# Kernel tuning notes

Hardware: AMD Instinct MI355X
Metric: run time of the kernel (lower is better)

The kernel has to match this reference:

```python
import jax, jax.numpy as jnp
import numpy as np

N, E, G = 100000, 300000, 4096
ND, ED, H, ZI, ZS, NE, L = 64, 16, 256, 128, 128, 8, 3
LAMBDA_GRL = 1.0


def setup_inputs() -> dict:
    key = jax.random.key(0)
    ks = iter(jax.random.split(key, 64))
    def nrm(shape, scale=0.05):
        return jax.random.normal(next(ks), shape, jnp.float32) * scale
    inp = {
        'x': jax.random.normal(next(ks), (N, ND), jnp.float32),
        'edge_index': jax.random.randint(next(ks), (2, E), 0, N),
        'edge_attr': jax.random.normal(next(ks), (E, ED), jnp.float32),
        'batch': jnp.sort(jax.random.randint(next(ks), (N,), 0, G)),
        'node_W': nrm((ND, H)), 'node_b': nrm((H,)),
        'conv_eps': jnp.zeros((L,), jnp.float32),
        'edge_W': nrm((L, ED, H)), 'edge_b': nrm((L, H)),
        'mlp_W1': nrm((L, H, H)), 'mlp_b1': nrm((L, H)),
        'mlp_W2': nrm((L, H, H)), 'mlp_b2': nrm((L, H)),
        'gn_w': jnp.ones((L, H), jnp.float32), 'gn_b': jnp.zeros((L, H), jnp.float32),
        'gn_ms': jnp.ones((L, H), jnp.float32),
        'finv_W1': nrm((H, ZI)), 'finv_b1': nrm((ZI,)),
        'finv_W2': nrm((ZI, ZI)), 'finv_b2': nrm((ZI,)),
        'fspu_W1': nrm((H, ZS)), 'fspu_b1': nrm((ZS,)),
        'fspu_W2': nrm((ZS, ZS)), 'fspu_b2': nrm((ZS,)),
        'pred_W1': nrm((ZI, ZI)), 'pred_b1': nrm((ZI,)),
        'pred_W2': nrm((ZI, 1)), 'pred_b2': nrm((1,)),
        'adv_W1': nrm((ZI, ZI)), 'adv_b1': nrm((ZI,)),
        'adv_W2': nrm((ZI, NE)), 'adv_b2': nrm((NE,)),
    }
    return inp


def _mlp2(h, W1, b1, W2, b2):
    return jax.nn.relu(h @ W1 + b1) @ W2 + b2


def reference(x, edge_index, edge_attr, batch, node_W, node_b, conv_eps,
              edge_W, edge_b, mlp_W1, mlp_b1, mlp_W2, mlp_b2,
              gn_w, gn_b, gn_ms,
              finv_W1, finv_b1, finv_W2, finv_b2,
              fspu_W1, fspu_b1, fspu_W2, fspu_b2,
              pred_W1, pred_b1, pred_W2, pred_b2,
              adv_W1, adv_b1, adv_W2, adv_b2):
    src, dst = edge_index[0], edge_index[1]
    cnt = jax.ops.segment_sum(jnp.ones((N, 1), jnp.float32), batch, num_segments=G)
    cnt = jnp.maximum(cnt, 1.0)
    h = x @ node_W + node_b  # [N,H]
    for l in range(L):
        # GINEConv: sum_j relu(x_j + lin(e_ij))
        e = edge_attr @ edge_W[l] + edge_b[l]            # [E,H]
        m = jax.nn.relu(h[src] + e)                      # [E,H]
        agg = jax.ops.segment_sum(m, dst, num_segments=N)
        h = _mlp2((1.0 + conv_eps[l]) * h + agg, mlp_W1[l], mlp_b1[l], mlp_W2[l], mlp_b2[l])
        # GraphNorm
        mean = jax.ops.segment_sum(h, batch, num_segments=G) / cnt  # [G,H]
        out = h - gn_ms[l] * mean[batch]
        var = jax.ops.segment_sum(out * out, batch, num_segments=G) / cnt
        h = out * jax.lax.rsqrt(var[batch] + 1e-5) * gn_w[l] + gn_b[l]
        h = jax.nn.relu(h)  # dropout is identity at eval
    hg = jax.ops.segment_sum(h, batch, num_segments=G) / cnt  # global_mean_pool [G,H]
    z_inv = _mlp2(hg, finv_W1, finv_b1, finv_W2, finv_b2)
    z_spu = _mlp2(hg, fspu_W1, fspu_b1, fspu_W2, fspu_b2)
    yhat = _mlp2(z_inv, pred_W1, pred_b1, pred_W2, pred_b2)[:, 0]
    # gradient reversal: identity fwd, -lambda on bwd
    grl = jax.lax.stop_gradient(z_inv) * (1.0 + LAMBDA_GRL) - LAMBDA_GRL * z_inv
    envhat = _mlp2(grl, adv_W1, adv_b1, adv_W2, adv_b2)
    return (hg, z_inv, z_spu, yhat, envhat)
```

## Files before the change

kernel.cpp:

```cpp
#include <hip/hip_runtime.h>
#include <hip/hip_bf16.h>

typedef __bf16 bf16_t;
typedef __bf16 bf16x8 __attribute__((ext_vector_type(8)));
typedef __bf16 bf16x4 __attribute__((ext_vector_type(4)));
typedef float  f32x4  __attribute__((ext_vector_type(4)));

static constexpr int N_NODES = 100000;
static constexpr int N_EDGES = 300000;
static constexpr int N_GRAPH = 4096;
static constexpr int H  = 256;
static constexpr int ND = 64;
static constexpr int ZIC = 128;
static constexpr int NE = 8;
static constexpr int SCAN_B = 1024;

__device__ __forceinline__ int clampi(int v, int lo, int hi) {
  return v < lo ? lo : (v > hi ? hi : v);
}

__device__ __forceinline__ void dma16(const bf16_t* g, bf16_t* lds_base) {
  __builtin_amdgcn_global_load_lds(
      (const __attribute__((address_space(1))) void*)g,
      (__attribute__((address_space(3))) void*)lds_base, 16, 0, 0);
}

__global__ void compute_starts_kernel(const int* __restrict__ batch,
                                      int* __restrict__ starts, int N, int G) {
  int i = blockIdx.x * blockDim.x + threadIdx.x;
  if (i >= N) return;
  int b = clampi(batch[i], 0, G - 1);
  if (i == 0) {
    for (int g = 0; g <= b; ++g) starts[g] = 0;
  } else {
    int p = clampi(batch[i - 1], 0, G - 1);
    for (int g = p + 1; g <= b; ++g) starts[g] = i;
  }
  if (i == N - 1) {
    for (int g = b + 1; g <= G; ++g) starts[g] = N;
  }
}

__global__ void zero2_kernel(int* __restrict__ a, int* __restrict__ b, int N) {
  int i = blockIdx.x * blockDim.x + threadIdx.x;
  if (i < N) { a[i] = 0; b[i] = 0; }
}

__global__ void count_deg_kernel(const int* __restrict__ dst, int* __restrict__ counts, int E, int N) {
  int e = blockIdx.x * blockDim.x + threadIdx.x;
  if (e < E) atomicAdd(&counts[clampi(dst[e], 0, N - 1)], 1);
}

__global__ __launch_bounds__(SCAN_B) void scan1_kernel(const int* __restrict__ counts,
                                                       int* __restrict__ offs,
                                                       int* __restrict__ bsum, int N) {
  __shared__ int tmp[SCAN_B];
  int i = blockIdx.x * SCAN_B + threadIdx.x;
  int v = (i < N) ? counts[i] : 0;
  tmp[threadIdx.x] = v;
  __syncthreads();
  for (int d = 1; d < SCAN_B; d <<= 1) {
    int t = (threadIdx.x >= d) ? tmp[threadIdx.x - d] : 0;
    __syncthreads();
    tmp[threadIdx.x] += t;
    __syncthreads();
  }
  if (i < N) offs[i + 1] = tmp[threadIdx.x];
  if (threadIdx.x == SCAN_B - 1) bsum[blockIdx.x] = tmp[SCAN_B - 1];
  if (i == 0) offs[0] = 0;
}

__global__ void scan2_kernel(int* __restrict__ bsum, int nblk) {
  if (blockIdx.x == 0 && threadIdx.x == 0) {
    int run = 0;
    for (int b = 0; b < nblk; ++b) { int v = bsum[b]; bsum[b] = run; run += v; }
  }
}

__global__ __launch_bounds__(SCAN_B) void scan3_kernel(int* __restrict__ offs,
                                                       const int* __restrict__ bsum, int N) {
  int i = blockIdx.x * SCAN_B + threadIdx.x;
  if (i < N) offs[i + 1] += bsum[blockIdx.x];
}

__global__ void fill_scatter_kernel(const int* __restrict__ src, const int* __restrict__ dst,
                                    const float* __restrict__ eattr,
                                    const int* __restrict__ offs, int* __restrict__ cursor,
                                    int* __restrict__ src_srt, bf16_t* __restrict__ eat16,
                                    int E, int N) {
  int e = blockIdx.x * blockDim.x + threadIdx.x;
  if (e >= E) return;
  int d = clampi(dst[e], 0, N - 1);
  int pos = offs[d] + atomicAdd(&cursor[d], 1);
  if ((unsigned)pos >= (unsigned)E) return;
  int s = src[e];
  src_srt[pos] = ((unsigned)s < (unsigned)N_NODES) ? s : 0;
  const float* ea = eattr + (size_t)e * 16;
  union { bf16_t b[16]; uint4 u[2]; } pk;
#pragma unroll
  for (int k = 0; k < 16; ++k) pk.b[k] = (bf16_t)ea[k];
  uint4* dst16 = (uint4*)(eat16 + ((size_t)pos << 4));
  dst16[0] = pk.u[0];
  dst16[1] = pk.u[1];
}

__global__ void build_ewt16_kernel(const float* __restrict__ edge_W,
                                   bf16_t* __restrict__ ewt) {
  int idx = blockIdx.x * blockDim.x + threadIdx.x;
  if (idx >= 3 * 256 * 16) return;
  int l = idx / (256 * 16);
  int rem = idx - l * 256 * 16;
  int n = rem >> 4, k = rem & 15;
  ewt[idx] = (bf16_t)edge_W[(size_t)l * 16 * 256 + k * 256 + n];
}

__global__ void transpose_kernel(const float* __restrict__ W,
                                 bf16_t* __restrict__ Wt, int K, int Nc,
                                 size_t srcStride, size_t dstStride) {
  __shared__ float tile[32][33];
  const float* Wz = W + (size_t)blockIdx.z * srcStride;
  bf16_t* Wtz = Wt + (size_t)blockIdx.z * dstStride;
  int n0 = blockIdx.x * 32, k0 = blockIdx.y * 32;
  int tx = threadIdx.x, ty = threadIdx.y;
  for (int i = ty; i < 32; i += 8)
    tile[i][tx] = Wz[(size_t)(k0 + i) * Nc + n0 + tx];
  __syncthreads();
  for (int i = ty; i < 32; i += 8)
    Wtz[(size_t)(n0 + i) * K + k0 + tx] = (bf16_t)tile[tx][i];
}

__device__ __forceinline__ void load8_to_lds(const bf16_t* p, bool valid, uint4* dst) {
  uint4 v = make_uint4(0u, 0u, 0u, 0u);
  if (valid) v = *(const uint4*)p;
  *dst = v;
}
__device__ __forceinline__ void load8_to_lds(const float* p, bool valid, uint4* dst) {
  float4 f0 = make_float4(0.f, 0.f, 0.f, 0.f), f1 = f0;
  if (valid) { f0 = *(const float4*)p; f1 = *(const float4*)(p + 4); }
  union { bf16_t b[8]; uint4 u; } pk;
  pk.b[0] = (bf16_t)f0.x; pk.b[1] = (bf16_t)f0.y;
  pk.b[2] = (bf16_t)f0.z; pk.b[3] = (bf16_t)f0.w;
  pk.b[4] = (bf16_t)f1.x; pk.b[5] = (bf16_t)f1.y;
  pk.b[6] = (bf16_t)f1.z; pk.b[7] = (bf16_t)f1.w;
  *dst = pk.u;
}

template<int K, bool RELU, bool OUTF32, typename TIN>
__global__ __launch_bounds__(256) void gemm128_kernel(
    const TIN* __restrict__ U, const bf16_t* __restrict__ Wt,
    const float* __restrict__ bias, void* __restrict__ Out, int M, int Nc) {
  constexpr int LDT = 72;
  __shared__ bf16_t Ut[128 * LDT];
  __shared__ bf16_t Wl[128 * LDT];
  const int m0 = blockIdx.x * 128;
  const int n0 = blockIdx.y * 128;
  const int t = threadIdx.x;
  const int lane = t & 63;
  const int wave = t >> 6;
  const int wm = (wave >> 1) * 64;
  const int wn = (wave & 1) * 64;
  const int srow = t >> 1;
  const int sk = (t & 1) * 32;
  const int lr = lane & 15;
  const int lq = lane >> 4;
  const bool aok = (m0 + srow) < M;
  f32x4 acc[4][4] = {};

  for (int k0 = 0; k0 < K; k0 += 64) {
    const TIN* up = U + (size_t)(m0 + srow) * K + k0 + sk;
    const bf16_t* wp = Wt + (size_t)(n0 + srow) * K + k0 + sk;
#pragma unroll
    for (int q = 0; q < 4; ++q) {
      load8_to_lds(up + q * 8, aok, (uint4*)&Ut[srow * LDT + sk + q * 8]);
      load8_to_lds(wp + q * 8, true, (uint4*)&Wl[srow * LDT + sk + q * 8]);
    }
    __syncthreads();
#pragma unroll
    for (int s = 0; s < 2; ++s) {
      bf16x8 a[4], b[4];
#pragma unroll
      for (int mt = 0; mt < 4; ++mt)
        a[mt] = *(const bf16x8*)(&Ut[(wm + mt * 16 + lr) * LDT + s * 32 + lq * 8]);
#pragma unroll
      for (int nt = 0; nt < 4; ++nt)
        b[nt] = *(const bf16x8*)(&Wl[(wn + nt * 16 + lr) * LDT + s * 32 + lq * 8]);
#pragma unroll
      for (int mt = 0; mt < 4; ++mt)
#pragma unroll
        for (int nt = 0; nt < 4; ++nt)
          acc[mt][nt] = __builtin_amdgcn_mfma_f32_16x16x32_bf16(
              a[mt], b[nt], acc[mt][nt], 0, 0, 0);
    }
    __syncthreads();
  }

#pragma unroll
  for (int mt = 0; mt < 4; ++mt)
#pragma unroll
    for (int nt = 0; nt < 4; ++nt) {
      int col = n0 + wn + nt * 16 + lr;
      float bcol = bias[col];
#pragma unroll
      for (int r = 0; r < 4; ++r) {
        int row = m0 + wm + mt * 16 + lq * 4 + r;
        if (row < M) {
          float vv = acc[mt][nt][r] + bcol;
          if (RELU) vv = vv > 0.f ? vv : 0.f;
          if (OUTF32) ((float*)Out)[(size_t)row * Nc + col] = vv;
          else        ((bf16_t*)Out)[(size_t)row * Nc + col] = (bf16_t)vv;
        }
      }
    }
}

template<int K, bool RELU, bool OUTF32, typename TIN>
__global__ __launch_bounds__(256) void gemm64_kernel(
    const TIN* __restrict__ U, const bf16_t* __restrict__ Wt,
    const float* __restrict__ bias, void* __restrict__ Out, int M, int Nc) {
  constexpr int LDT = 72;
  __shared__ bf16_t Ut[64 * LDT];
  __shared__ bf16_t Wl[64 * LDT];
  const int m0 = blockIdx.x * 64;
  const int n0 = blockIdx.y * 64;
  const int t = threadIdx.x;
  const int lane = t & 63;
  const int wave = t >> 6;
  const int wm = (wave >> 1) * 32;
  const int wn = (wave & 1) * 32;
  const int srow = t >> 2;
  const int sk = (t & 3) * 8;
  const int lr = lane & 15;
  const int lq = lane >> 4;
  const bool aok = (m0 + srow) < M;
  f32x4 acc[2][2] = {};

  for (int k0 = 0; k0 < K; k0 += 64) {
    const TIN* up = U + (size_t)(m0 + srow) * K + k0 + sk;
    const bf16_t* wp = Wt + (size_t)(n0 + srow) * K + k0 + sk;
    load8_to_lds(up,      aok, (uint4*)&Ut[srow * LDT + sk]);
    load8_to_lds(up + 32, aok, (uint4*)&Ut[srow * LDT + sk + 32]);
    load8_to_lds(wp,      true, (uint4*)&Wl[srow * LDT + sk]);
    load8_to_lds(wp + 32, true, (uint4*)&Wl[srow * LDT + sk + 32]);
    __syncthreads();
#pragma unroll
    for (int s = 0; s < 2; ++s) {
      bf16x8 a[2], b[2];
#pragma unroll
      for (int mt = 0; mt < 2; ++mt)
        a[mt] = *(const bf16x8*)(&Ut[(wm + mt * 16 + lr) * LDT + s * 32 + lq * 8]);
#pragma unroll
      for (int nt = 0; nt < 2; ++nt)
        b[nt] = *(const bf16x8*)(&Wl[(wn + nt * 16 + lr) * LDT + s * 32 + lq * 8]);
#pragma unroll
      for (int mt = 0; mt < 2; ++mt)
#pragma unroll
        for (int nt = 0; nt < 2; ++nt)
          acc[mt][nt] = __builtin_amdgcn_mfma_f32_16x16x32_bf16(
              a[mt], b[nt], acc[mt][nt], 0, 0, 0);
    }
    __syncthreads();
  }

#pragma unroll
  for (int mt = 0; mt < 2; ++mt)
#pragma unroll
    for (int nt = 0; nt < 2; ++nt) {
      int col = n0 + wn + nt * 16 + lr;
      float bcol = bias[col];
#pragma unroll
      for (int r = 0; r < 4; ++r) {
        int row = m0 + wm + mt * 16 + lq * 4 + r;
        if (row < M) {
          float vv = acc[mt][nt][r] + bcol;
          if (RELU) vv = vv > 0.f ? vv : 0.f;
          if (OUTF32) ((float*)Out)[(size_t)row * Nc + col] = vv;
          else        ((bf16_t*)Out)[(size_t)row * Nc + col] = (bf16_t)vv;
        }
      }
    }
}

template<int K, bool RELU, bool OUTF32>
__global__ __launch_bounds__(256) void gemm128_dma_kernel(
    const bf16_t* __restrict__ U, const bf16_t* __restrict__ Wt,
    const float* __restrict__ bias, void* __restrict__ Out, int M, int Nc) {
  __shared__ bf16_t Ut[128 * 64];
  __shared__ bf16_t Wl[128 * 64];
  const int t = threadIdx.x;
  const int lane = t & 63;
  const int wave = t >> 6;
  const int m0 = blockIdx.x * 128;
  const int n0 = blockIdx.y * 128;
  const int wm = (wave >> 1) * 64;
  const int wn = (wave & 1) * 64;
  const int lr = lane & 15;
  const int lq = lane >> 4;
  const int subrow = wave * 8 + (lane >> 3);
  const int lchunk = (lane & 7) ^ (lane >> 3);
  f32x4 acc[4][4] = {};

  for (int k0 = 0; k0 < K; k0 += 64) {
#pragma unroll
    for (int q = 0; q < 4; ++q) {
      const int row = q * 32 + subrow;
      int urow = m0 + row; if (urow >= M) urow = M - 1;
      dma16(U + (size_t)urow * K + k0 + lchunk * 8, &Ut[(q * 32 + wave * 8) * 64]);
      dma16(Wt + (size_t)(n0 + row) * K + k0 + lchunk * 8, &Wl[(q * 32 + wave * 8) * 64]);
    }
    __syncthreads();
#pragma unroll
    for (int s = 0; s < 2; ++s) {
      bf16x8 a[4], b[4];
#pragma unroll
      for (int mt = 0; mt < 4; ++mt)
        a[mt] = *(const bf16x8*)(&Ut[(wm + mt * 16 + lr) * 64 + (((s * 4 + lq) ^ (lr & 7)) << 3)]);
#pragma unroll
      for (int nt = 0; nt < 4; ++nt)
        b[nt] = *(const bf16x8*)(&Wl[(wn + nt * 16 + lr) * 64 + (((s * 4 + lq) ^ (lr & 7)) << 3)]);
#pragma unroll
      for (int mt = 0; mt < 4; ++mt)
#pragma unroll
        for (int nt = 0; nt < 4; ++nt)
          acc[mt][nt] = __builtin_amdgcn_mfma_f32_16x16x32_bf16(
              a[mt], b[nt], acc[mt][nt], 0, 0, 0);
    }
    __syncthreads();
  }

#pragma unroll
  for (int mt = 0; mt < 4; ++mt)
#pragma unroll
    for (int nt = 0; nt < 4; ++nt) {
      int col = n0 + wn + nt * 16 + lr;
      float bcol = bias[col];
#pragma unroll
      for (int r = 0; r < 4; ++r) {
        int row = m0 + wm + mt * 16 + lq * 4 + r;
        if (row < M) {
          float vv = acc[mt][nt][r] + bcol;
          if (RELU) vv = vv > 0.f ? vv : 0.f;
          if (OUTF32) ((float*)Out)[(size_t)row * Nc + col] = vv;
          else        ((bf16_t*)Out)[(size_t)row * Nc + col] = (bf16_t)vv;
        }
      }
    }
}

__global__ __launch_bounds__(256) void gine_gather_mfma_kernel(
    const bf16_t* __restrict__ h, const bf16_t* __restrict__ eat16,
    const int* __restrict__ src_sorted, const int* __restrict__ offs,
    const bf16_t* __restrict__ ewt, const float* __restrict__ eb,
    const float* __restrict__ eps_p, bf16_t* __restrict__ u) {
  constexpr int HP = H + 8;
  __shared__ bf16_t slin[2][16 * HP];
  const int t = threadIdx.x;
  const int wave = t >> 6;
  const int lane = t & 63;
  const int lr = lane & 15;
  const int lq = lane >> 4;
  const int lane4 = lane * 4;
  const int n0 = blockIdx.x * 4;
  const int nodeN = n0 + wave;

  bf16x4 hs = *(const bf16x4*)(h + (size_t)nodeN * H + lane4);

  bf16x8 bfrag[4];
#pragma unroll
  for (int nt = 0; nt < 4; ++nt) {
    bf16x8 bv = {};
    if (lq < 2)
      bv = *(const bf16x8*)(ewt + ((wave * 64 + nt * 16 + lr) << 4) + (lq << 3));
    bfrag[nt] = bv;
  }
  float ebv[4];
#pragma unroll
  for (int i = 0; i < 4; ++i) ebv[i] = eb[lane4 + i];

  int bs = offs[n0], be = offs[n0 + 4];
  bs = clampi(bs, 0, N_EDGES);
  be = clampi(be, bs, N_EDGES);
  int ns = offs[nodeN], ne = offs[nodeN + 1];
  ns = clampi(ns, bs, be);
  ne = clampi(ne, ns, be);

  float acc[4] = {0.f, 0.f, 0.f, 0.f};
  int parity = 0;

  for (int cb = bs; cb < be; cb += 16, parity ^= 1) {
    int arow = cb + lr;
    if (arow >= N_EDGES) arow = N_EDGES - 1;
    bf16x8 afrag = {};
    if (lq < 2)
      afrag = *(const bf16x8*)(eat16 + ((size_t)arow << 4) + (lq << 3));
    f32x4 c[4];
#pragma unroll
    for (int nt = 0; nt < 4; ++nt) {
      f32x4 z = {};
      c[nt] = __builtin_amdgcn_mfma_f32_16x16x32_bf16(afrag, bfrag[nt], z, 0, 0, 0);
    }
#pragma unroll
    for (int nt = 0; nt < 4; ++nt)
#pragma unroll
      for (int r = 0; r < 4; ++r)
        slin[parity][(lq * 4 + r) * HP + wave * 64 + nt * 16 + lr] = (bf16_t)c[nt][r];
    __syncthreads();
    int j0 = ns > cb ? ns : cb;
    int j1 = ne < cb + 16 ? ne : cb + 16;
    for (int jb = j0; jb < j1; jb += 4) {
      int sidx[4];
#pragma unroll
      for (int q = 0; q < 4; ++q) {
        int jj = jb + q; if (jj > j1 - 1) jj = j1 - 1;
        sidx[q] = src_sorted[jj];
      }
      bf16x4 hv[4];
#pragma unroll
      for (int q = 0; q < 4; ++q)
        hv[q] = *(const bf16x4*)(h + (size_t)sidx[q] * H + lane4);
#pragma unroll
      for (int q = 0; q < 4; ++q) {
        if (jb + q < j1) {
          bf16x4 lv = *(const bf16x4*)(&slin[parity][(jb + q - cb) * HP + lane4]);
#pragma unroll
          for (int i = 0; i < 4; ++i)
            acc[i] += fmaxf((float)hv[q][i] + (float)lv[i] + ebv[i], 0.f);
        }
      }
    }
  }

  const float sc = 1.0f + eps_p[0];
  union { bf16x4 v; uint2 b; } o;
#pragma unroll
  for (int i = 0; i < 4; ++i) o.v[i] = (bf16_t)(sc * (float)hs[i] + acc[i]);
  *(uint2*)(u + (size_t)nodeN * H + lane4) = o.b;
}

__global__ __launch_bounds__(64) void graphnorm_kernel(
    const bf16_t* __restrict__ v, bf16_t* __restrict__ hout,
    const int* __restrict__ starts,
    const float* __restrict__ w, const float* __restrict__ b,
    const float* __restrict__ ms, float* __restrict__ hg) {
  const int g = blockIdx.x;
  const int c0 = threadIdx.x * 4;
  int s = starts[g], e = starts[g + 1];
  s = clampi(s, 0, N_NODES);
  e = clampi(e, s, N_NODES);
  const float cnt = (float)((e - s) > 1 ? (e - s) : 1);
  float sx[4] = {0.f, 0.f, 0.f, 0.f}, sxx[4] = {0.f, 0.f, 0.f, 0.f};
  int i = s;
  for (; i + 4 <= e; i += 4) {
    bf16x4 xv[4];
#pragma unroll
    for (int q = 0; q < 4; ++q)
      xv[q] = *(const bf16x4*)(v + (size_t)(i + q) * H + c0);
#pragma unroll
    for (int q = 0; q < 4; ++q)
#pragma unroll
      for (int j = 0; j < 4; ++j) { float f = (float)xv[q][j]; sx[j] += f; sxx[j] += f * f; }
  }
  for (; i < e; ++i) {
    bf16x4 xv = *(const bf16x4*)(v + (size_t)i * H + c0);
#pragma unroll
    for (int j = 0; j < 4; ++j) { float f = (float)xv[j]; sx[j] += f; sxx[j] += f * f; }
  }
  float sub[4], inv[4], bb[4], psum[4] = {0.f, 0.f, 0.f, 0.f};
#pragma unroll
  for (int j = 0; j < 4; ++j) {
    float mean = sx[j] / cnt;
    sub[j] = ms[c0 + j] * mean;
    float var = sxx[j] / cnt - 2.f * sub[j] * mean + sub[j] * sub[j];
    var = fmaxf(var, 0.f);
    inv[j] = rsqrtf(var + 1e-5f) * w[c0 + j];
    bb[j] = b[c0 + j];
  }
  i = s;
  for (; i + 4 <= e; i += 4) {
    bf16x4 xv[4];
#pragma unroll
    for (int q = 0; q < 4; ++q)
      xv[q] = *(const bf16x4*)(v + (size_t)(i + q) * H + c0);
#pragma unroll
    for (int q = 0; q < 4; ++q) {
      union { bf16x4 o; uint2 u; } pk;
#pragma unroll
      for (int j = 0; j < 4; ++j) {
        float o = ((float)xv[q][j] - sub[j]) * inv[j] + bb[j];
        o = o > 0.f ? o : 0.f;
        psum[j] += o;
        pk.o[j] = (bf16_t)o;
      }
      *(uint2*)(hout + (size_t)(i + q) * H + c0) = pk.u;
    }
  }
  for (; i < e; ++i) {
    bf16x4 xv = *(const bf16x4*)(v + (size_t)i * H + c0);
    union { bf16x4 o; uint2 u; } pk;
#pragma unroll
    for (int j = 0; j < 4; ++j) {
      float o = ((float)xv[j] - sub[j]) * inv[j] + bb[j];
      o = o > 0.f ? o : 0.f;
      psum[j] += o;
      pk.o[j] = (bf16_t)o;
    }
    *(uint2*)(hout + (size_t)i * H + c0) = pk.u;
  }
  if (hg) {
#pragma unroll
    for (int j = 0; j < 4; ++j) hg[(size_t)g * H + c0 + j] = psum[j] / cnt;
  }
}

__global__ void head_out_kernel(const bf16_t* __restrict__ In, const float* __restrict__ W,
                                const float* __restrict__ bias, float* __restrict__ Out,
                                int M, int K, int Nc) {
  int idx = blockIdx.x * blockDim.x + threadIdx.x;
  if (idx >= M * Nc) return;
  int r = idx / Nc, n = idx - r * Nc;
  float acc = bias[n];
  const bf16_t* in = In + (size_t)r * K;
  for (int k = 0; k < K; ++k) acc += (float)in[k] * W[(size_t)k * Nc + n];
  Out[idx] = acc;
}

extern "C" void kernel_launch(void* const* d_in, const int* in_sizes, int n_in,
                              void* d_out, int out_size, void* d_ws, size_t ws_size,
                              hipStream_t stream) {
  (void)in_sizes; (void)n_in; (void)out_size; (void)ws_size;
  const float* x        = (const float*)d_in[0];
  const int*   eidx     = (const int*)d_in[1];
  const float* eattr    = (const float*)d_in[2];
  const int*   batch    = (const int*)d_in[3];
  const float* node_W   = (const float*)d_in[4];
  const float* node_b   = (const float*)d_in[5];
  const float* conv_eps = (const float*)d_in[6];
  const float* edge_W   = (const float*)d_in[7];
  const float* edge_b   = (const float*)d_in[8];
  const float* mlp_W1   = (const float*)d_in[9];
  const float* mlp_b1   = (const float*)d_in[10];
  const float* mlp_W2   = (const float*)d_in[11];
  const float* mlp_b2   = (const float*)d_in[12];
  const float* gn_w     = (const float*)d_in[13];
  const float* gn_b     = (const float*)d_in[14];
  const float* gn_ms    = (const float*)d_in[15];
  const float* finv_W1  = (const float*)d_in[16];
  const float* finv_b1  = (const float*)d_in[17];
  const float* finv_W2  = (const float*)d_in[18];
  const float* finv_b2  = (const float*)d_in[19];
  const float* fspu_W1  = (const float*)d_in[20];
  const float* fspu_b1  = (const float*)d_in[21];
  const float* fspu_W2  = (const float*)d_in[22];
  const float* fspu_b2  = (const float*)d_in[23];
  const float* pred_W1  = (const float*)d_in[24];
  const float* pred_b1  = (const float*)d_in[25];
  const float* pred_W2  = (const float*)d_in[26];
  const float* pred_b2  = (const float*)d_in[27];
  const float* adv_W1   = (const float*)d_in[28];
  const float* adv_b1   = (const float*)d_in[29];
  const float* adv_W2   = (const float*)d_in[30];
  const float* adv_b2   = (const float*)d_in[31];
  float* out = (float*)d_out;

  float* out_hg = out;
  float* out_zi = out + (size_t)N_GRAPH * H;
  float* out_zs = out_zi + (size_t)N_GRAPH * ZIC;
  float* out_yh = out_zs + (size_t)N_GRAPH * ZIC;
  float* out_ev = out_yh + N_GRAPH;

  char* wp = (char*)d_ws;
  auto alloc = [&](size_t bytes) { char* p = wp; wp += (bytes + 255) & ~(size_t)255; return p; };
  bf16_t* A        = (bf16_t*)alloc((size_t)N_NODES * H * 2);
  bf16_t* B        = (bf16_t*)alloc((size_t)N_NODES * H * 2);
  bf16_t* Wt       = (bf16_t*)alloc((size_t)(H * ND + 6 * H * H) * 2);
  bf16_t* WtH      = (bf16_t*)alloc((size_t)(2 * ZIC * H + 4 * ZIC * ZIC) * 2);
  bf16_t* ewt16    = (bf16_t*)alloc((size_t)3 * 256 * 16 * 2);
  bf16_t* eat16    = (bf16_t*)alloc((size_t)N_EDGES * 16 * 2);
  int*    starts   = (int*)alloc((size_t)(N_GRAPH + 1) * 4);
  int*    counts   = (int*)alloc((size_t)N_NODES * 4);
  int*    cursor   = (int*)alloc((size_t)N_NODES * 4);
  int*    offs     = (int*)alloc((size_t)(N_NODES + 1) * 4);
  int*    bsum     = (int*)alloc((size_t)SCAN_B * 4);
  int*    src_srt  = (int*)alloc((size_t)N_EDGES * 4);
  bf16_t* tmp1     = (bf16_t*)alloc((size_t)N_GRAPH * ZIC * 2);
  bf16_t* tmp2     = (bf16_t*)alloc((size_t)N_GRAPH * ZIC * 2);

  const int* srcp = eidx;
  const int* dstp = eidx + N_EDGES;
  const int nscan = (N_NODES + SCAN_B - 1) / SCAN_B;

  compute_starts_kernel<<<(N_NODES + 255) / 256, 256, 0, stream>>>(batch, starts, N_NODES, N_GRAPH);

  zero2_kernel<<<(N_NODES + 255) / 256, 256, 0, stream>>>(counts, cursor, N_NODES);
  count_deg_kernel<<<(N_EDGES + 255) / 256, 256, 0, stream>>>(dstp, counts, N_EDGES, N_NODES);
  scan1_kernel<<<nscan, SCAN_B, 0, stream>>>(counts, offs, bsum, N_NODES);
  scan2_kernel<<<1, 64, 0, stream>>>(bsum, nscan);
  scan3_kernel<<<nscan, SCAN_B, 0, stream>>>(offs, bsum, N_NODES);
  fill_scatter_kernel<<<(N_EDGES + 255) / 256, 256, 0, stream>>>(
      srcp, dstp, eattr, offs, cursor, src_srt, eat16, N_EDGES, N_NODES);
  build_ewt16_kernel<<<(3 * 256 * 16 + 255) / 256, 256, 0, stream>>>(edge_W, ewt16);

  bf16_t* WtN = Wt;
  bf16_t* Wt1base = Wt + H * ND;
  bf16_t* Wt2base = Wt + H * ND + (size_t)H * H;
  auto Wt1l = [&](int l) { return Wt1base + (size_t)(2 * l) * H * H; };
  auto Wt2l = [&](int l) { return Wt2base + (size_t)(2 * l) * H * H; };
  transpose_kernel<<<dim3(H / 32, ND / 32, 1), dim3(32, 8), 0, stream>>>(node_W, WtN, ND, H, 0, 0);
  transpose_kernel<<<dim3(H / 32, H / 32, 3), dim3(32, 8), 0, stream>>>(
      mlp_W1, Wt1base, H, H, (size_t)H * H, (size_t)2 * H * H);
  transpose_kernel<<<dim3(H / 32, H / 32, 3), dim3(32, 8), 0, stream>>>(
      mlp_W2, Wt2base, H, H, (size_t)H * H, (size_t)2 * H * H);

  bf16_t* fT1 = WtH;
  bf16_t* fT2 = fT1 + ZIC * H;
  bf16_t* sT1 = fT2 + ZIC * ZIC;
  bf16_t* sT2 = sT1 + ZIC * H;
  bf16_t* pT1 = sT2 + ZIC * ZIC;
  bf16_t* aT1 = pT1 + ZIC * ZIC;
  transpose_kernel<<<dim3(ZIC / 32, H / 32, 1), dim3(32, 8), 0, stream>>>(finv_W1, fT1, H, ZIC, 0, 0);
  transpose_kernel<<<dim3(ZIC / 32, ZIC / 32, 1), dim3(32, 8), 0, stream>>>(finv_W2, fT2, ZIC, ZIC, 0, 0);
  transpose_kernel<<<dim3(ZIC / 32, H / 32, 1), dim3(32, 8), 0, stream>>>(fspu_W1, sT1, H, ZIC, 0, 0);
  transpose_kernel<<<dim3(ZIC / 32, ZIC / 32, 1), dim3(32, 8), 0, stream>>>(fspu_W2, sT2, ZIC, ZIC, 0, 0);
  transpose_kernel<<<dim3(ZIC / 32, ZIC / 32, 1), dim3(32, 8), 0, stream>>>(pred_W1, pT1, ZIC, ZIC, 0, 0);
  transpose_kernel<<<dim3(ZIC / 32, ZIC / 32, 1), dim3(32, 8), 0, stream>>>(adv_W1, aT1, ZIC, ZIC, 0, 0);

  dim3 ggrid((N_NODES + 127) / 128, H / 128);
  gemm128_kernel<ND, false, false><<<ggrid, 256, 0, stream>>>(x, WtN, node_b, A, N_NODES, H);

  for (int l = 0; l < 3; ++l) {
    gine_gather_mfma_kernel<<<N_NODES / 4, 256, 0, stream>>>(
        A, eat16, src_srt, offs, ewt16 + (size_t)l * 256 * 16,
        edge_b + l * H, conv_eps + l, B);
    gemm128_dma_kernel<H, true,  false><<<ggrid, 256, 0, stream>>>(B, Wt1l(l), mlp_b1 + l * H, A, N_NODES, H);
    gemm128_dma_kernel<H, false, false><<<ggrid, 256, 0, stream>>>(A, Wt2l(l), mlp_b2 + l * H, B, N_NODES, H);
    graphnorm_kernel<<<N_GRAPH, 64, 0, stream>>>(B, A, starts, gn_w + l * H, gn_b + l * H,
                                                 gn_ms + l * H, (l == 2) ? out_hg : nullptr);
  }

  dim3 hgrid(N_GRAPH / 64, ZIC / 64);
  gemm64_kernel<H,   true,  false, float ><<<hgrid, 256, 0, stream>>>(out_hg, fT1, finv_b1, tmp1, N_GRAPH, ZIC);
  gemm64_kernel<ZIC, false, true,  bf16_t><<<hgrid, 256, 0, stream>>>(tmp1, fT2, finv_b2, out_zi, N_GRAPH, ZIC);
  gemm64_kernel<H,   true,  false, float ><<<hgrid, 256, 0, stream>>>(out_hg, sT1, fspu_b1, tmp2, N_GRAPH, ZIC);
  gemm64_kernel<ZIC, false, true,  bf16_t><<<hgrid, 256, 0, stream>>>(tmp2, sT2, fspu_b2, out_zs, N_GRAPH, ZIC);
  gemm64_kernel<ZIC, true,  false, float ><<<hgrid, 256, 0, stream>>>(out_zi, pT1, pred_b1, tmp1, N_GRAPH, ZIC);
  gemm64_kernel<ZIC, true,  false, float ><<<hgrid, 256, 0, stream>>>(out_zi, aT1, adv_b1, tmp2, N_GRAPH, ZIC);
  head_out_kernel<<<(N_GRAPH + 255) / 256, 256, 0, stream>>>(tmp1, pred_W2, pred_b2, out_yh, N_GRAPH, ZIC, 1);
  head_out_kernel<<<(N_GRAPH * NE + 255) / 256, 256, 0, stream>>>(tmp2, adv_W2, adv_b2, out_ev, N_GRAPH, ZIC, NE);
}
```

Baseline: 817.1 us.

## Fuse per-layer two-GEMM MLP into one kernel and batch head GEMMs

Replaces the two separate 128x128-tiled GEMM launches per GIN layer with a single fused kernel. Each 64-row tile is loaded into LDS once, the first GEMM plus ReLU is computed and written back to LDS, and the second GEMM runs on that tile, so the hidden activation never goes through global memory. Weights are read straight from global memory rather than staged in LDS, which may raise L2 traffic or latency. It also folds the counter zeroing into compute_starts, parallelizes the block-sum scan, and concatenates the head weight matrices so fewer small GEMM launches are needed.

```diff
diff --git a/kernel.cpp b/kernel.cpp
--- a/kernel.cpp
+++ b/kernel.cpp
@@ -19,16 +19,14 @@
   return v < lo ? lo : (v > hi ? hi : v);
 }
 
-__device__ __forceinline__ void dma16(const bf16_t* g, bf16_t* lds_base) {
-  __builtin_amdgcn_global_load_lds(
-      (const __attribute__((address_space(1))) void*)g,
-      (__attribute__((address_space(3))) void*)lds_base, 16, 0, 0);
-}
-
 __global__ void compute_starts_kernel(const int* __restrict__ batch,
-                                      int* __restrict__ starts, int N, int G) {
+                                      int* __restrict__ starts,
+                                      int* __restrict__ counts,
+                                      int* __restrict__ cursor, int N, int G) {
   int i = blockIdx.x * blockDim.x + threadIdx.x;
   if (i >= N) return;
+  counts[i] = 0;
+  cursor[i] = 0;
   int b = clampi(batch[i], 0, G - 1);
   if (i == 0) {
     for (int g = 0; g <= b; ++g) starts[g] = 0;
@@ -39,11 +37,6 @@
   if (i == N - 1) {
     for (int g = b + 1; g <= G; ++g) starts[g] = N;
   }
-}
-
-__global__ void zero2_kernel(int* __restrict__ a, int* __restrict__ b, int N) {
-  int i = blockIdx.x * blockDim.x + threadIdx.x;
-  if (i < N) { a[i] = 0; b[i] = 0; }
 }
 
 __global__ void count_deg_kernel(const int* __restrict__ dst, int* __restrict__ counts, int E, int N) {
@@ -70,11 +63,19 @@
   if (i == 0) offs[0] = 0;
 }
 
-__global__ void scan2_kernel(int* __restrict__ bsum, int nblk) {
-  if (blockIdx.x == 0 && threadIdx.x == 0) {
-    int run = 0;
-    for (int b = 0; b < nblk; ++b) { int v = bsum[b]; bsum[b] = run; run += v; }
-  }
+__global__ __launch_bounds__(128) void scan2_kernel(int* __restrict__ bsum, int nblk) {
+  __shared__ int tmp[128];
+  int t = threadIdx.x;
+  int v = (t < nblk) ? bsum[t] : 0;
+  tmp[t] = v;
+  __syncthreads();
+  for (int d = 1; d < 128; d <<= 1) {
+    int x = (t >= d) ? tmp[t - d] : 0;
+    __syncthreads();
+    tmp[t] += x;
+    __syncthreads();
+  }
+  if (t < nblk) bsum[t] = tmp[t] - v;
 }
 
 __global__ __launch_bounds__(SCAN_B) void scan3_kernel(int* __restrict__ offs,
@@ -213,10 +214,101 @@
     }
 }
 
+__global__ __launch_bounds__(256) void fused_mlp_kernel(
+    const bf16_t* __restrict__ U, const bf16_t* __restrict__ W1t,
+    const float* __restrict__ b1, const bf16_t* __restrict__ W2t,
+    const float* __restrict__ b2, bf16_t* __restrict__ V, int M) {
+  constexpr int LDT = 264;
+  __shared__ bf16_t T[64 * LDT];
+  const int t = threadIdx.x;
+  const int lane = t & 63;
+  const int wave = t >> 6;
+  const int m0 = blockIdx.x * 64;
+  const int lr = lane & 15;
+  const int lq = lane >> 4;
+  const int wn = wave * 64;
+
+  {
+    int row = t >> 2;
+    int cbase = (t & 3) * 64;
+    int grow = m0 + row; if (grow >= M) grow = M - 1;
+    const bf16_t* src = U + (size_t)grow * 256 + cbase;
+#pragma unroll
+    for (int c = 0; c < 8; ++c)
+      *(uint4*)&T[row * LDT + cbase + c * 8] = *(const uint4*)(src + c * 8);
+  }
+  __syncthreads();
+
+  f32x4 acc[4][4] = {};
+#pragma unroll
+  for (int ks = 0; ks < 8; ++ks) {
+    const int k0 = ks * 32;
+    bf16x8 a[4], b[4];
+#pragma unroll
+    for (int mt = 0; mt < 4; ++mt)
+      a[mt] = *(const bf16x8*)&T[(mt * 16 + lr) * LDT + k0 + lq * 8];
+#pragma unroll
+    for (int nt = 0; nt < 4; ++nt)
+      b[nt] = *(const bf16x8*)(W1t + (size_t)(wn + nt * 16 + lr) * 256 + k0 + lq * 8);
+#pragma unroll
+    for (int mt = 0; mt < 4; ++mt)
+#pragma unroll
+      for (int nt = 0; nt < 4; ++nt)
+        acc[mt][nt] = __builtin_amdgcn_mfma_f32_16x16x32_bf16(
+            a[mt], b[nt], acc[mt][nt], 0, 0, 0);
+  }
+  __syncthreads();
+#pragma unroll
+  for (int nt = 0; nt < 4; ++nt) {
+    float bc = b1[wn + nt * 16 + lr];
+#pragma unroll
+    for (int mt = 0; mt < 4; ++mt)
+#pragma unroll
+      for (int r = 0; r < 4; ++r) {
+        float vv = acc[mt][nt][r] + bc;
+        vv = vv > 0.f ? vv : 0.f;
+        T[(mt * 16 + lq * 4 + r) * LDT + wn + nt * 16 + lr] = (bf16_t)vv;
+      }
+  }
+  __syncthreads();
+
+  f32x4 acc2[4][4] = {};
+#pragma unroll
+  for (int ks = 0; ks < 8; ++ks) {
+    const int k0 = ks * 32;
+    bf16x8 a[4], b[4];
+#pragma unroll
+    for (int mt = 0; mt < 4; ++mt)
+      a[mt] = *(const bf16x8*)&T[(mt * 16 + lr) * LDT + k0 + lq * 8];
+#pragma unroll
+    for (int nt = 0; nt < 4; ++nt)
+      b[nt] = *(const bf16x8*)(W2t + (size_t)(wn + nt * 16 + lr) * 256 + k0 + lq * 8);
+#pragma unroll
+    for (int mt = 0; mt < 4; ++mt)
+#pragma unroll
+      for (int nt = 0; nt < 4; ++nt)
+        acc2[mt][nt] = __builtin_amdgcn_mfma_f32_16x16x32_bf16(
+            a[mt], b[nt], acc2[mt][nt], 0, 0, 0);
+  }
+#pragma unroll
+  for (int nt = 0; nt < 4; ++nt) {
+    float bc = b2[wn + nt * 16 + lr];
+#pragma unroll
+    for (int mt = 0; mt < 4; ++mt)
+#pragma unroll
+      for (int r = 0; r < 4; ++r) {
+        int row = m0 + mt * 16 + lq * 4 + r;
+        if (row < M)
+          V[(size_t)row * 256 + wn + nt * 16 + lr] = (bf16_t)(acc2[mt][nt][r] + bc);
+      }
+  }
+}
+
 template<int K, bool RELU, bool OUTF32, typename TIN>
 __global__ __launch_bounds__(256) void gemm64_kernel(
-    const TIN* __restrict__ U, const bf16_t* __restrict__ Wt,
-    const float* __restrict__ bias, void* __restrict__ Out, int M, int Nc) {
+    const TIN* __restrict__ U, int lda, const bf16_t* __restrict__ Wt,
+    const float* __restrict__ bias0, const float* __restrict__ bias1, int bsplit,
+    void* __restrict__ Out, int ldo, int M) {
   constexpr int LDT = 72;
   __shared__ bf16_t Ut[64 * LDT];
   __shared__ bf16_t Wl[64 * LDT];
@@ -235,7 +327,7 @@
   f32x4 acc[2][2] = {};
 
   for (int k0 = 0; k0 < K; k0 += 64) {
-    const TIN* up = U + (size_t)(m0 + srow) * K + k0 + sk;
+    const TIN* up = U + (size_t)(m0 + srow) * lda + k0 + sk;
     const bf16_t* wp = Wt + (size_t)(n0 + srow) * K + k0 + sk;
     load8_to_lds(up,      aok, (uint4*)&Ut[srow * LDT + sk]);
     load8_to_lds(up + 32, aok, (uint4*)&Ut[srow * LDT + sk + 32]);
@@ -266,81 +358,15 @@
 #pragma unroll
     for (int nt = 0; nt < 2; ++nt) {
       int col = n0 + wn + nt * 16 + lr;
-      float bcol = bias[col];
+      float bcol = (col < bsplit) ? bias0[col] : bias1[col - bsplit];
 #pragma unroll
       for (int r = 0; r < 4; ++r) {
         int row = m0 + wm + mt * 16 + lq * 4 + r;
         if (row < M) {
           float vv = acc[mt][nt][r] + bcol;
           if (RELU) vv = vv > 0.f ? vv : 0.f;
-          if (OUTF32) ((float*)Out)[(size_t)row * Nc + col] = vv;
-          else        ((bf16_t*)Out)[(size_t)row * Nc + col] = (bf16_t)vv;
-        }
-      }
-    }
-}
-
-template<int K, bool RELU, bool OUTF32>
-__global__ __launch_bounds__(256) void gemm128_dma_kernel(
-    const bf16_t* __restrict__ U, const bf16_t* __restrict__ Wt,
-    const float* __restrict__ bias, void* __restrict__ Out, int M, int Nc) {
-  __shared__ bf16_t Ut[128 * 64];
-  __shared__ bf16_t Wl[128 * 64];
-  const int t = threadIdx.x;
-  const int lane = t & 63;
-  const int wave = t >> 6;
-  const int m0 = blockIdx.x * 128;
-  const int n0 = blockIdx.y * 128;
-  const int wm = (wave >> 1) * 64;
-  const int wn = (wave & 1) * 64;
-  const int lr = lane & 15;
-  const int lq = lane >> 4;
-  const int subrow = wave * 8 + (lane >> 3);
-  const int lchunk = (lane & 7) ^ (lane >> 3);
-  f32x4 acc[4][4] = {};
-
-  for (int k0 = 0; k0 < K; k0 += 64) {
-#pragma unroll
-    for (int q = 0; q < 4; ++q) {
-      const int row = q * 32 + subrow;
-      int urow = m0 + row; if (urow >= M) urow = M - 1;
-      dma16(U + (size_t)urow * K + k0 + lchunk * 8, &Ut[(q * 32 + wave * 8) * 64]);
-      dma16(Wt + (size_t)(n0 + row) * K + k0 + lchunk * 8, &Wl[(q * 32 + wave * 8) * 64]);
-    }
-    __syncthreads();
-#pragma unroll
-    for (int s = 0; s < 2; ++s) {
-      bf16x8 a[4], b[4];
-#pragma unroll
-      for (int mt = 0; mt < 4; ++mt)
-        a[mt] = *(const bf16x8*)(&Ut[(wm + mt * 16 + lr) * 64 + (((s * 4 + lq) ^ (lr & 7)) << 3)]);
-#pragma unroll
-      for (int nt = 0; nt < 4; ++nt)
-        b[nt] = *(const bf16x8*)(&Wl[(wn + nt * 16 + lr) * 64 + (((s * 4 + lq) ^ (lr & 7)) << 3)]);
-#pragma unroll
-      for (int mt = 0; mt < 4; ++mt)
-#pragma unroll
-        for (int nt = 0; nt < 4; ++nt)
-          acc[mt][nt] = __builtin_amdgcn_mfma_f32_16x16x32_bf16(
-              a[mt], b[nt], acc[mt][nt], 0, 0, 0);
-    }
-    __syncthreads();
-  }
-
-#pragma unroll
-  for (int mt = 0; mt < 4; ++mt)
-#pragma unroll
-    for (int nt = 0; nt < 4; ++nt) {
-      int col = n0 + wn + nt * 16 + lr;
-      float bcol = bias[col];
-#pragma unroll
-      for (int r = 0; r < 4; ++r) {
-        int row = m0 + wm + mt * 16 + lq * 4 + r;
-        if (row < M) {
-          float vv = acc[mt][nt][r] + bcol;
-          if (RELU) vv = vv > 0.f ? vv : 0.f;
-          if (OUTF32) ((float*)Out)[(size_t)row * Nc + col] = vv;
-          else        ((bf16_t*)Out)[(size_t)row * Nc + col] = (bf16_t)vv;
+          if (OUTF32) ((float*)Out)[(size_t)row * ldo + col] = vv;
+          else        ((bf16_t*)Out)[(size_t)row * ldo + col] = (bf16_t)vv;
         }
       }
     }
@@ -511,14 +537,15 @@
   }
 }
 
-__global__ void head_out_kernel(const bf16_t* __restrict__ In, const float* __restrict__ W,
+__global__ void head_out_kernel(const bf16_t* __restrict__ In, int lda,
+                                const float* __restrict__ W,
                                 const float* __restrict__ bias, float* __restrict__ Out,
                                 int M, int K, int Nc) {
   int idx = blockIdx.x * blockDim.x + threadIdx.x;
   if (idx >= M * Nc) return;
   int r = idx / Nc, n = idx - r * Nc;
   float acc = bias[n];
-  const bf16_t* in = In + (size_t)r * K;
+  const bf16_t* in = In + (size_t)r * lda;
   for (int k = 0; k < K; ++k) acc += (float)in[k] * W[(size_t)k * Nc + n];
   Out[idx] = acc;
 }
@@ -581,19 +608,18 @@
   int*    offs     = (int*)alloc((size_t)(N_NODES + 1) * 4);
   int*    bsum     = (int*)alloc((size_t)SCAN_B * 4);
   int*    src_srt  = (int*)alloc((size_t)N_EDGES * 4);
-  bf16_t* tmp1     = (bf16_t*)alloc((size_t)N_GRAPH * ZIC * 2);
-  bf16_t* tmp2     = (bf16_t*)alloc((size_t)N_GRAPH * ZIC * 2);
+  bf16_t* tmp12    = (bf16_t*)alloc((size_t)N_GRAPH * 2 * ZIC * 2);
+  bf16_t* tmp34    = (bf16_t*)alloc((size_t)N_GRAPH * 2 * ZIC * 2);
 
   const int* srcp = eidx;
   const int* dstp = eidx + N_EDGES;
   const int nscan = (N_NODES + SCAN_B - 1) / SCAN_B;
 
-  compute_starts_kernel<<<(N_NODES + 255) / 256, 256, 0, stream>>>(batch, starts, N_NODES, N_GRAPH);
-
-  zero2_kernel<<<(N_NODES + 255) / 256, 256, 0, stream>>>(counts, cursor, N_NODES);
+  compute_starts_kernel<<<(N_NODES + 255) / 256, 256, 0, stream>>>(
+      batch, starts, counts, cursor, N_NODES, N_GRAPH);
   count_deg_kernel<<<(N_EDGES + 255) / 256, 256, 0, stream>>>(dstp, counts, N_EDGES, N_NODES);
   scan1_kernel<<<nscan, SCAN_B, 0, stream>>>(counts, offs, bsum, N_NODES);
-  scan2_kernel<<<1, 64, 0, stream>>>(bsum, nscan);
+  scan2_kernel<<<1, 128, 0, stream>>>(bsum, nscan);
   scan3_kernel<<<nscan, SCAN_B, 0, stream>>>(offs, bsum, N_NODES);
   fill_scatter_kernel<<<(N_EDGES + 255) / 256, 256, 0, stream>>>(
       srcp, dstp, eattr, offs, cursor, src_srt, eat16, N_EDGES, N_NODES);
@@ -610,39 +636,42 @@
   transpose_kernel<<<dim3(H / 32, H / 32, 3), dim3(32, 8), 0, stream>>>(
       mlp_W2, Wt2base, H, H, (size_t)H * H, (size_t)2 * H * H);
 
-  bf16_t* fT1 = WtH;
-  bf16_t* fT2 = fT1 + ZIC * H;
-  bf16_t* sT1 = fT2 + ZIC * ZIC;
-  bf16_t* sT2 = sT1 + ZIC * H;
-  bf16_t* pT1 = sT2 + ZIC * ZIC;
-  bf16_t* aT1 = pT1 + ZIC * ZIC;
-  transpose_kernel<<<dim3(ZIC / 32, H / 32, 1), dim3(32, 8), 0, stream>>>(finv_W1, fT1, H, ZIC, 0, 0);
+  bf16_t* cat1 = WtH;
+  bf16_t* fT2  = cat1 + 256 * 256;
+  bf16_t* sT2  = fT2 + ZIC * ZIC;
+  bf16_t* cat2 = sT2 + ZIC * ZIC;
+  transpose_kernel<<<dim3(ZIC / 32, H / 32, 1), dim3(32, 8), 0, stream>>>(finv_W1, cat1, H, ZIC, 0, 0);
+  transpose_kernel<<<dim3(ZIC / 32, H / 32, 1), dim3(32, 8), 0, stream>>>(fspu_W1, cat1 + (size_t)ZIC * H, H, ZIC, 0, 0);
   transpose_kernel<<<dim3(ZIC / 32, ZIC / 32, 1), dim3(32, 8), 0, stream>>>(finv_W2, fT2, ZIC, ZIC, 0, 0);
-  transpose_kernel<<<dim3(ZIC / 32, H / 32, 1), dim3(32, 8), 0, stream>>>(fspu_W1, sT1, H, ZIC, 0, 0);
   transpose_kernel<<<dim3(ZIC / 32, ZIC / 32, 1), dim3(32, 8), 0, stream>>>(fspu_W2, sT2, ZIC, ZIC, 0, 0);
-  transpose_kernel<<<dim3(ZIC / 32, ZIC / 32, 1), dim3(32, 8), 0, stream>>>(pred_W1, pT1, ZIC, ZIC, 0, 0);
-  transpose_kernel<<<dim3(ZIC / 32, ZIC / 32, 1), dim3(32, 8), 0, stream>>>(adv_W1, aT1, ZIC, ZIC, 0, 0);
+  transpose_kernel<<<dim3(ZIC / 32, ZIC / 32, 1), dim3(32, 8), 0, stream>>>(pred_W1, cat2, ZIC, ZIC, 0, 0);
+  transpose_kernel<<<dim3(ZIC / 32, ZIC / 32, 1), dim3(32, 8), 0, stream>>>(adv_W1, cat2 + (size_t)ZIC * ZIC, ZIC, ZIC, 0, 0);
 
   dim3 ggrid((N_NODES + 127) / 128, H / 128);
   gemm128_kernel<ND, false, false><<<ggrid, 256, 0, stream>>>(x, WtN, node_b, A, N_NODES, H);
 
+  const int nmlp = (N_NODES + 63) / 64;
   for (int l = 0; l < 3; ++l) {
     gine_gather_mfma_kernel<<<N_NODES / 4, 256, 0, stream>>>(
         A, eat16, src_srt, offs, ewt16 + (size_t)l * 256 * 16,
         edge_b + l * H, conv_eps + l, B);
-    gemm128_dma_kernel<H, true,  false><<<ggrid, 256, 0, stream>>>(B, Wt1l(l), mlp_b1 + l * H, A, N_NODES, H);
-    gemm128_dma_kernel<H, false, false><<<ggrid, 256, 0, stream>>>(A, Wt2l(l), mlp_b2 + l * H, B, N_NODES, H);
+    fused_mlp_kernel<<<nmlp, 256, 0, stream>>>(
+        B, Wt1l(l), mlp_b1 + l * H, Wt2l(l), mlp_b2 + l * H, B, N_NODES);
     graphnorm_kernel<<<N_GRAPH, 64, 0, stream>>>(B, A, starts, gn_w + l * H, gn_b + l * H,
                                                  gn_ms + l * H, (l == 2) ? out_hg : nullptr);
   }
 
-  dim3 hgrid(N_GRAPH / 64, ZIC / 64);
-  gemm64_kernel<H,   true,  false, float ><<<hgrid, 256, 0, stream>>>(out_hg, fT1, finv_b1, tmp1, N_GRAPH, ZIC);
-  gemm64_kernel<ZIC, false, true,  bf16_t><<<hgrid, 256, 0, stream>>>(tmp1, fT2, finv_b2, out_zi, N_GRAPH, ZIC);
-  gemm64_kernel<H,   true,  false, float ><<<hgrid, 256, 0, stream>>>(out_hg, sT1, fspu_b1, tmp2, N_GRAPH, ZIC);
-  gemm64_kernel<ZIC, false, true,  bf16_t><<<hgrid, 256, 0, stream>>>(tmp2, sT2, fspu_b2, out_zs, N_GRAPH, ZIC);
-  gemm64_kernel<ZIC, true,  false, float ><<<hgrid, 256, 0, stream>>>(out_zi, pT1, pred_b1, tmp1, N_GRAPH, ZIC);
-  gemm64_kernel<ZIC, true,  false, float ><<<hgrid, 256, 0, stream>>>(out_zi, aT1, adv_b1, tmp2, N_GRAPH, ZIC);
-  head_out_kernel<<<(N_GRAPH + 255) / 256, 256, 0, stream>>>(tmp1, pred_W2, pred_b2, out_yh, N_GRAPH, ZIC, 1);
-  head_out_kernel<<<(N_GRAPH * NE + 255) / 256, 256, 0, stream>>>(tmp2, adv_W2, adv_b2, out_ev, N_GRAPH, ZIC, NE);
-}
+  const int BIG = 1 << 30;
+  gemm64_kernel<H,   true,  false, float ><<<dim3(N_GRAPH / 64, 4), 256, 0, stream>>>(
+      out_hg, H, cat1, finv_b1, fspu_b1, ZIC, tmp12, 2 * ZIC, N_GRAPH);
+  gemm64_kernel<ZIC, false, true,  bf16_t><<<dim3(N_GRAPH / 64, 2), 256, 0, stream>>>(
+      tmp12, 2 * ZIC, fT2, finv_b2, finv_b2, BIG, out_zi, ZIC, N_GRAPH);
+  gemm64_kernel<ZIC, false, true,  bf16_t><<<dim3(N_GRAPH / 64, 2), 256, 0, stream>>>(
+      tmp12 + ZIC, 2 * ZIC, sT2, fspu_b2, fspu_b2, BIG, out_zs, ZIC, N_GRAPH);
+  gemm64_kernel<ZIC, true,  false, float ><<<dim3(N_GRAPH / 64, 4), 256, 0, stream>>>(
+      out_zi, ZIC, cat2, pred_b1, adv_b1, ZIC, tmp34, 2 * ZIC, N_GRAPH);
+  head_out_kernel<<<(N_GRAPH + 255) / 256, 256, 0, stream>>>(
+      tmp34, 2 * ZIC, pred_W2, pred_b2, out_yh, N_GRAPH, ZIC, 1);
+  head_out_kernel<<<(N_GRAPH * NE + 255) / 256, 256, 0, stream>>>(
+      tmp34 + ZIC, 2 * ZIC, adv_W2, adv_b2, out_ev, N_GRAPH, ZIC, NE);
+}
```

After: 852.6 us. +4.3%, slower.
